# Kernel tuning notes

Measured on AMD Instinct MI355X. Metric: run time of the kernel, lower is better.

## Reference

```python
import jax, jax.numpy as jnp
import numpy as np

C = 512

def _conv1x1(x, w, b):
    # x: [B, C, T], w: [O, C], b: [O] -> [B, O, T]
    return jnp.einsum('oc,bct->bot', w, x) + b[None, :, None]

def setup_inputs() -> dict:
    key = jax.random.key(0)
    ks = jax.random.split(key, 9)
    B, T = 8, 2048
    s = 1.0 / np.sqrt(C)
    inp = {'x': jax.random.normal(ks[0], (B, C, T), dtype=jnp.float32)}
    names = ['theta', 'phi', 'g', 'w']
    for i, n in enumerate(names):
        inp[f'w_{n}'] = jax.random.uniform(ks[1 + 2 * i], (C, C), jnp.float32, -s, s)
        inp[f'b_{n}'] = jax.random.uniform(ks[2 + 2 * i], (C,), jnp.float32, -s, s)
    return inp

def reference(x, w_theta, b_theta, w_phi, b_phi, w_g, b_g, w_w, b_w):
    relu = jax.nn.relu
    feat_theta = relu(_conv1x1(x, w_theta, b_theta))          # [B, C, T]
    feat_phi = relu(_conv1x1(x, w_phi, b_phi))                # [B, C, T]
    # scores: Q^T K over channel dim -> [B, T, T]
    scores = jnp.einsum('bci,bcj->bij', feat_theta, feat_phi)
    attn = jax.nn.softmax(scores, axis=2)                     # [B, T, T]
    feat_g = relu(_conv1x1(x, w_g, b_g))                      # [B, C, T]
    # attention-weighted V: [B, T, T] x [B, T, C] -> [B, T, C] -> [B, C, T]
    feature = jnp.einsum('bij,bcj->bci', attn, feat_g)
    w_feature = relu(_conv1x1(feature, w_w, b_w))
    return w_feature + x
```

## Files before the change

kernel.cpp:

```cpp
#include <hip/hip_runtime.h>
#include <math.h>

#define C_DIM 512
#define T_DIM 2048
#define B_DIM 8

typedef _Float16 f16;
typedef __attribute__((ext_vector_type(8))) _Float16 half8;
typedef __attribute__((ext_vector_type(4))) _Float16 half4;
typedef __attribute__((ext_vector_type(4))) float floatx4;

__global__ __launch_bounds__(256) void convert_w_kernel(
    const float* __restrict__ w0, const float* __restrict__ w1,
    const float* __restrict__ w2, const float* __restrict__ w3,
    f16* __restrict__ o0, f16* __restrict__ o1,
    f16* __restrict__ o2, f16* __restrict__ o3)
{
    const float* src; f16* dst;
    switch (blockIdx.z) {
        case 0:  src = w0; dst = o0; break;
        case 1:  src = w1; dst = o1; break;
        case 2:  src = w2; dst = o2; break;
        default: src = w3; dst = o3; break;
    }
    const int idx = (blockIdx.x * 256 + threadIdx.x) * 4;
    const float4 v = *(const float4*)(src + idx);
    half4 h; h[0] = (f16)v.x; h[1] = (f16)v.y; h[2] = (f16)v.z; h[3] = (f16)v.w;
    *(half4*)(dst + idx) = h;
}

__global__ __launch_bounds__(256) void concat_bias_kernel(
    const float* __restrict__ b0, const float* __restrict__ b1,
    float* __restrict__ o)
{
    const int i = blockIdx.x * 256 + threadIdx.x;
    o[i] = (i < 512) ? b0[i] : b1[i - 512];
}

__global__ __launch_bounds__(256) void transpose_x_kernel(
    const float* __restrict__ x, f16* __restrict__ xt)
{
    __shared__ float xs[32][33];
    const int b  = blockIdx.z;
    const int t0 = blockIdx.x * 32, c0 = blockIdx.y * 32;
    const float* xb = x + (size_t)b * C_DIM * T_DIM;
    const int r = threadIdx.x >> 3, q = threadIdx.x & 7;

    const float4 v = *(const float4*)(xb + (size_t)(c0 + r) * T_DIM + t0 + q * 4);
    xs[r][q * 4 + 0] = v.x; xs[r][q * 4 + 1] = v.y;
    xs[r][q * 4 + 2] = v.z; xs[r][q * 4 + 3] = v.w;
    __syncthreads();

    f16* xtb = xt + (size_t)b * C_DIM * T_DIM;
    half4 h;
    h[0] = (f16)xs[q * 4 + 0][r]; h[1] = (f16)xs[q * 4 + 1][r];
    h[2] = (f16)xs[q * 4 + 2][r]; h[3] = (f16)xs[q * 4 + 3][r];
    *(half4*)(xtb + (size_t)(t0 + r) * C_DIM + c0 + q * 4) = h;
}

__device__ __forceinline__ void gl16(const f16* g, f16* l)
{
    __builtin_amdgcn_global_load_lds(
        (const __attribute__((address_space(1))) unsigned int*)g,
        (__attribute__((address_space(3))) unsigned int*)l,
        16, 0, 0);
}


template<int MODE>
__global__ __launch_bounds__(512, 2) void gemm256(
    const f16* __restrict__ A, size_t sA, int lda,
    const f16* __restrict__ B, size_t sB, int ldb,
    void* __restrict__ Cp, size_t sC, int ldc,
    const float* __restrict__ bias,
    int gx, int K)
{
    __shared__ __align__(16) f16 As[2][2][256 * 32];
    __shared__ __align__(16) f16 Bs[2][2][256 * 32];

    const int f = blockIdx.x;
    const int bz = f & 7;
    const int flat = f >> 3;
    const int jsc = gx >> 2;
    const int sh = (jsc <= 1) ? 0 : (31 - __builtin_clz(jsc));
    const int s = flat >> 4, rem = flat & 15;
    const int i0 = ((s >> sh) * 4 + (rem >> 2)) * 256;
    const int j0 = (((jsc <= 1) ? 0 : (s & (jsc - 1))) * 4 + (rem & 3)) * 256;

    A += (size_t)bz * sA;
    B += (size_t)bz * sB;

    const int tid  = threadIdx.x;
    const int lane = tid & 63;
    const int wave = tid >> 6;
    const int wy = wave >> 2;
    const int wx = wave & 3;
    const int quad = lane >> 4, l16 = lane & 15;

    const int srow = wave * 32 + (lane >> 2);
    const int sch  = (lane & 3) ^ ((lane >> 3) & 3);
    const f16* gA0 = A + (size_t)(i0 + srow) * lda + sch * 8;
    const f16* gA1 = gA0 + (size_t)16 * lda;
    const f16* gB0 = B + (size_t)(j0 + srow) * ldb + sch * 8;
    const f16* gB1 = gB0 + (size_t)16 * ldb;
    const int wsg = wave * 1024;

    const int xq = (quad ^ ((l16 >> 1) & 3)) << 3;
    const int ra = (wy * 128 + l16) * 32 + xq;
    const int rb = (wx * 64 + l16) * 32 + xq;

    const int nt = K >> 6;

#define STAGE_A(t, q) do {                                                    \
        const int off_ = (t) * 64 + (q) * 32;                                 \
        gl16(gA0 + off_, &As[(t) & 1][q][wsg]);                               \
        gl16(gA1 + off_, &As[(t) & 1][q][wsg + 512]);                         \
    } while (0)
#define STAGE_B(t, q) do {                                                    \
        const int off_ = (t) * 64 + (q) * 32;                                 \
        gl16(gB0 + off_, &Bs[(t) & 1][q][wsg]);                               \
        gl16(gB1 + off_, &Bs[(t) & 1][q][wsg + 512]);                         \
    } while (0)
#define PH_MFMA(B0) do {                                                      \
        __builtin_amdgcn_s_setprio(1);                                        \
        _Pragma("unroll")                                                     \
        for (int mi = 0; mi < 4; ++mi) {                                      \
            _Pragma("unroll")                                                 \
            for (int ni = 0; ni < 4; ++ni)                                    \
                acc[(B0) + mi][ni] = __builtin_amdgcn_mfma_f32_16x16x32_f16(  \
                    af[mi], bf[ni], acc[(B0) + mi][ni], 0, 0, 0);             \
        }                                                                     \
        __builtin_amdgcn_s_setprio(0);                                        \
    } while (0)

    STAGE_A(0, 0); STAGE_B(0, 0);
    STAGE_A(0, 1); STAGE_B(0, 1);
    STAGE_A(1, 0); STAGE_B(1, 0);

    floatx4 acc[8][4] = {};

    for (int t = 0; t < nt; ++t) {
        const f16* sa0 = &As[t & 1][0][0];
        const f16* sb0 = &Bs[t & 1][0][0];
        const f16* sa1 = &As[t & 1][1][0];
        const f16* sb1 = &Bs[t & 1][1][0];
        half8 af[4], bf[4];

        if (t + 1 < nt) asm volatile("s_waitcnt vmcnt(8)\ns_barrier" ::: "memory");
        else            asm volatile("s_waitcnt vmcnt(4)\ns_barrier" ::: "memory");
        #pragma unroll
        for (int ni = 0; ni < 4; ++ni) bf[ni] = *(const half8*)&sb0[rb + ni * 512];
        #pragma unroll
        for (int mi = 0; mi < 4; ++mi) af[mi] = *(const half8*)&sa0[ra + mi * 512];
        if (t + 1 < nt) STAGE_A(t + 1, 1);
        PH_MFMA(0);

        #pragma unroll
        for (int mi = 0; mi < 4; ++mi) af[mi] = *(const half8*)&sa0[ra + 2048 + mi * 512];
        if (t + 1 < nt) STAGE_B(t + 1, 1);
        PH_MFMA(4);

        if (t + 1 < nt) asm volatile("s_waitcnt vmcnt(8)\ns_barrier" ::: "memory");
        else            asm volatile("s_waitcnt vmcnt(0)\ns_barrier" ::: "memory");
        #pragma unroll
        for (int ni = 0; ni < 4; ++ni) bf[ni] = *(const half8*)&sb1[rb + ni * 512];
        #pragma unroll
        for (int mi = 0; mi < 4; ++mi) af[mi] = *(const half8*)&sa1[ra + mi * 512];
        if (t + 2 < nt) STAGE_A(t + 2, 0);
        PH_MFMA(0);

        #pragma unroll
        for (int mi = 0; mi < 4; ++mi) af[mi] = *(const half8*)&sa1[ra + 2048 + mi * 512];
        if (t + 2 < nt) STAGE_B(t + 2, 0);
        PH_MFMA(4);
    }
#undef STAGE_A
#undef STAGE_B
#undef PH_MFMA

    #pragma unroll
    for (int m = 0; m < 8; ++m) {
        #pragma unroll
        for (int ni = 0; ni < 4; ++ni) {
            const int col = j0 + wx * 64 + ni * 16 + l16;
            #pragma unroll
            for (int r = 0; r < 4; ++r) {
                const int row = i0 + wy * 128 + m * 16 + quad * 4 + r;
                float v = acc[m][ni][r];
                if (MODE == 1) { v += bias[col]; v = v > 0.f ? v : 0.f; }
                ((f16*)Cp)[(size_t)bz * sC + (size_t)row * ldc + col] = (f16)v;
            }
        }
    }
}

template<int MODE>
__global__ __launch_bounds__(512, 2) void gemm_wide(
    const f16* __restrict__ A, size_t sA, int lda,
    const f16* __restrict__ B, size_t sB, int ldb,
    void* __restrict__ Cp, size_t sC, int ldc,
    const float* __restrict__ bias,
    const float* __restrict__ resid, size_t sR,
    int gxn, int K)
{
    __shared__ __align__(16) f16 As[2][2][128 * 32];
    __shared__ __align__(16) f16 Bs[2][2][256 * 32];

    const int f = blockIdx.x;
    const int bz = f & 7;
    const int inner = f >> 3;
    const int j0 = (inner % gxn) * 256;
    const int i0 = (inner / gxn) * 128;
    A += (size_t)bz * sA;
    B += (size_t)bz * sB;

    const int tid  = threadIdx.x;
    const int lane = tid & 63;
    const int wave = tid >> 6;
    const int wy = wave >> 2;
    const int wx = wave & 3;
    const int quad = lane >> 4, l16 = lane & 15;

    const int sch = (lane & 3) ^ ((lane >> 3) & 3);
    const f16* gA0 = A + (size_t)(i0 + wave * 16 + (lane >> 2)) * lda + sch * 8;
    const f16* gB0 = B + (size_t)(j0 + wave * 32 + (lane >> 2)) * ldb + sch * 8;
    const f16* gB1 = gB0 + (size_t)16 * ldb;

    const int xq = (quad ^ ((l16 >> 1) & 3)) << 3;
    const int ra = (wy * 64 + l16) * 32 + xq;
    const int rb = (wx * 64 + l16) * 32 + xq;

    const int nt = K >> 6;

#define WSTAGE_A(t, q) do {                                                   \
        gl16(gA0 + (t) * 64 + (q) * 32, &As[(t) & 1][q][wave * 512]);         \
    } while (0)
#define WSTAGE_B(t, q) do {                                                   \
        const int off_ = (t) * 64 + (q) * 32;                                 \
        gl16(gB0 + off_, &Bs[(t) & 1][q][wave * 1024]);                       \
        gl16(gB1 + off_, &Bs[(t) & 1][q][wave * 1024 + 512]);                 \
    } while (0)
#define WPH_MFMA() do {                                                       \
        __builtin_amdgcn_s_setprio(1);                                        \
        _Pragma("unroll")                                                     \
        for (int mi = 0; mi < 4; ++mi) {                                      \
            _Pragma("unroll")                                                 \
            for (int ni = 0; ni < 4; ++ni)                                    \
                acc[mi][ni] = __builtin_amdgcn_mfma_f32_16x16x32_f16(         \
                    af[mi], bf[ni], acc[mi][ni], 0, 0, 0);                    \
        }                                                                     \
        __builtin_amdgcn_s_setprio(0);                                        \
    } while (0)

    WSTAGE_A(0, 0); WSTAGE_B(0, 0);
    WSTAGE_A(0, 1); WSTAGE_B(0, 1);
    WSTAGE_A(1, 0); WSTAGE_B(1, 0);

    floatx4 acc[4][4] = {};

    for (int t = 0; t < nt; ++t) {
        const f16* sa0 = &As[t & 1][0][0];
        const f16* sb0 = &Bs[t & 1][0][0];
        const f16* sa1 = &As[t & 1][1][0];
        const f16* sb1 = &Bs[t & 1][1][0];
        half8 af[4], bf[4];

        if (t + 1 < nt) asm volatile("s_waitcnt vmcnt(6)\ns_barrier" ::: "memory");
        else            asm volatile("s_waitcnt vmcnt(3)\ns_barrier" ::: "memory");
        #pragma unroll
        for (int ni = 0; ni < 4; ++ni) bf[ni] = *(const half8*)&sb0[rb + ni * 512];
        #pragma unroll
        for (int mi = 0; mi < 4; ++mi) af[mi] = *(const half8*)&sa0[ra + mi * 512];
        if (t + 1 < nt) { WSTAGE_A(t + 1, 1); WSTAGE_B(t + 1, 1); }
        WPH_MFMA();

        if (t + 1 < nt) asm volatile("s_waitcnt vmcnt(6)\ns_barrier" ::: "memory");
        else            asm volatile("s_waitcnt vmcnt(0)\ns_barrier" ::: "memory");
        #pragma unroll
        for (int ni = 0; ni < 4; ++ni) bf[ni] = *(const half8*)&sb1[rb + ni * 512];
        #pragma unroll
        for (int mi = 0; mi < 4; ++mi) af[mi] = *(const half8*)&sa1[ra + mi * 512];
        if (t + 2 < nt) { WSTAGE_A(t + 2, 0); WSTAGE_B(t + 2, 0); }
        WPH_MFMA();
    }
#undef WSTAGE_A
#undef WSTAGE_B
#undef WPH_MFMA

    #pragma unroll
    for (int mi = 0; mi < 4; ++mi) {
        #pragma unroll
        for (int ni = 0; ni < 4; ++ni) {
            const int col = j0 + wx * 64 + ni * 16 + l16;
            #pragma unroll
            for (int r = 0; r < 4; ++r) {
                const int row = i0 + wy * 64 + mi * 16 + quad * 4 + r;
                float v = acc[mi][ni][r];
                if (MODE == 2) { v += bias[row]; v = v > 0.f ? v : 0.f; }
                if (MODE == 3) {
                    v += bias[row];
                    v = v > 0.f ? v : 0.f;
                    v += resid[(size_t)bz * sR + (size_t)row * ldc + col];
                    ((float*)Cp)[(size_t)bz * sC + (size_t)row * ldc + col] = v;
                } else {
                    ((f16*)Cp)[(size_t)bz * sC + (size_t)row * ldc + col] = (f16)v;
                }
            }
        }
    }
}

__global__ __launch_bounds__(256) void softmax_f16_kernel(f16* __restrict__ S)
{
    const int lane = threadIdx.x & 63;
    f16* p = S + (size_t)(blockIdx.x * 4 + (threadIdx.x >> 6)) * T_DIM;

    half8 h[4];
    float v[32];
    float m = -1e30f;
    #pragma unroll
    for (int u = 0; u < 4; ++u) {
        h[u] = *((const half8*)p + (u * 64 + lane));
        #pragma unroll
        for (int c = 0; c < 8; ++c) {
            v[u * 8 + c] = (float)h[u][c];
            m = fmaxf(m, v[u * 8 + c]);
        }
    }
    #pragma unroll
    for (int off = 32; off; off >>= 1) m = fmaxf(m, __shfl_xor(m, off));

    float s = 0.f;
    #pragma unroll
    for (int i = 0; i < 32; ++i) { v[i] = __expf(v[i] - m); s += v[i]; }
    #pragma unroll
    for (int off = 32; off; off >>= 1) s += __shfl_xor(s, off);
    const float inv = 1.f / s;

    #pragma unroll
    for (int u = 0; u < 4; ++u) {
        #pragma unroll
        for (int c = 0; c < 8; ++c) h[u][c] = (f16)(v[u * 8 + c] * inv);
        *((half8*)p + (u * 64 + lane)) = h[u];
    }
}

extern "C" void kernel_launch(void* const* d_in, const int* in_sizes, int n_in,
                              void* d_out, int out_size, void* d_ws, size_t ws_size,
                              hipStream_t stream)
{
    const float* x       = (const float*)d_in[0];
    const float* w_theta = (const float*)d_in[1];
    const float* b_theta = (const float*)d_in[2];
    const float* w_phi   = (const float*)d_in[3];
    const float* b_phi   = (const float*)d_in[4];
    const float* w_g     = (const float*)d_in[5];
    const float* b_g     = (const float*)d_in[6];
    const float* w_w     = (const float*)d_in[7];
    const float* b_w     = (const float*)d_in[8];
    float* out = (float*)d_out;

    const size_t FE = (size_t)B_DIM * C_DIM * T_DIM;
    const size_t TC = (size_t)T_DIM * C_DIM;
    const size_t TT = (size_t)T_DIM * T_DIM;

    f16* xt      = (f16*)d_ws;
    f16* wtp     = xt + FE;
    f16* wg_h    = wtp + 524288;
    f16* ww_h    = wg_h + 262144;
    float* btp   = (float*)(ww_h + 262144);
    f16* tp      = (f16*)(btp + 1024);
    f16* g       = tp + (size_t)B_DIM * T_DIM * 1024;
    f16* scores  = g + FE;
    f16* feature = tp;

    const dim3 blk(256);
    const dim3 blk512(512);

    convert_w_kernel<<<dim3(256, 1, 4), blk, 0, stream>>>(
        w_theta, w_phi, w_g, w_w, wtp, wtp + 262144, wg_h, ww_h);
    concat_bias_kernel<<<dim3(4), blk, 0, stream>>>(b_theta, b_phi, btp);
    transpose_x_kernel<<<dim3(T_DIM / 32, C_DIM / 32, B_DIM), blk, 0, stream>>>(x, xt);

    gemm256<1><<<dim3(4 * 8 * B_DIM), blk512, 0, stream>>>(
        xt, TC, C_DIM, wtp, 0, C_DIM, tp, (size_t)T_DIM * 1024, 1024,
        btp, 4, C_DIM);
    gemm_wide<2><<<dim3(8 * 4 * B_DIM), blk512, 0, stream>>>(
        wg_h, 0, C_DIM, xt, TC, C_DIM, g, TC, T_DIM, b_g, nullptr, 0,
        8, C_DIM);
    gemm256<0><<<dim3(8 * 8 * B_DIM), blk512, 0, stream>>>(
        tp, (size_t)T_DIM * 1024, 1024, tp + 512, (size_t)T_DIM * 1024, 1024,
        scores, TT, T_DIM, nullptr, 8, C_DIM);
    softmax_f16_kernel<<<dim3(B_DIM * T_DIM / 4), blk, 0, stream>>>(scores);
    gemm_wide<0><<<dim3(2 * 16 * B_DIM), blk512, 0, stream>>>(
        scores, TT, T_DIM, g, TC, T_DIM, feature, TC, C_DIM,
        nullptr, nullptr, 0, 2, T_DIM);
    gemm_wide<3><<<dim3(8 * 4 * B_DIM), blk512, 0, stream>>>(
        ww_h, 0, C_DIM, feature, TC, C_DIM, out, TC, T_DIM, b_w, x, TC,
        8, C_DIM);
}
```

Measured before the change: 258.0 us.

## Fuse softmax into score GEMM epilogue and rescale in attention-V GEMM

Removes the separate softmax kernel. The score GEMM epilogue now computes a per-tile row max, writes exp(s - tile_max) as f16, and stores per-tile (max, sum) stats. The attention-V GEMM reads those stats, rescales each K-tile of A by exp(tile_max - global_max) through registers into LDS, and applies 1/l in its epilogue. This drops one full read and write of the B×T×T score matrix. In exchange, the A operand is staged through registers instead of direct global-to-LDS loads, adds extra vector-ALU work, reuses the wtp workspace for stats, and changes the pipeline wait counts.

```diff
diff --git a/kernel.cpp b/kernel.cpp
--- a/kernel.cpp
+++ b/kernel.cpp
@@ -73,6 +73,7 @@
     const f16* __restrict__ B, size_t sB, int ldb,
     void* __restrict__ Cp, size_t sC, int ldc,
     const float* __restrict__ bias,
+    float2* __restrict__ stats,
     int gx, int K)
 {
     __shared__ __align__(16) f16 As[2][2][256 * 32];
@@ -178,17 +179,73 @@
 #undef STAGE_B
 #undef PH_MFMA
 
-    #pragma unroll
-    for (int m = 0; m < 8; ++m) {
-        #pragma unroll
-        for (int ni = 0; ni < 4; ++ni) {
-            const int col = j0 + wx * 64 + ni * 16 + l16;
+    if constexpr (MODE == 2) {
+        float* red  = (float*)&As[0][0][0];
+        float* mr   = red + 1024;
+        float* red2 = mr + 256;
+        const int jb = j0 >> 8;
+
+        __syncthreads();
+        #pragma unroll
+        for (int m = 0; m < 8; ++m) {
             #pragma unroll
             for (int r = 0; r < 4; ++r) {
-                const int row = i0 + wy * 128 + m * 16 + quad * 4 + r;
-                float v = acc[m][ni][r];
-                if (MODE == 1) { v += bias[col]; v = v > 0.f ? v : 0.f; }
-                ((f16*)Cp)[(size_t)bz * sC + (size_t)row * ldc + col] = (f16)v;
+                float v = fmaxf(fmaxf(acc[m][0][r], acc[m][1][r]),
+                                fmaxf(acc[m][2][r], acc[m][3][r]));
+                v = fmaxf(v, __shfl_xor(v, 1));
+                v = fmaxf(v, __shfl_xor(v, 2));
+                v = fmaxf(v, __shfl_xor(v, 4));
+                v = fmaxf(v, __shfl_xor(v, 8));
+                if (l16 == 0)
+                    red[(wy * 128 + m * 16 + quad * 4 + r) * 4 + wx] = v;
+            }
+        }
+        __syncthreads();
+        if (tid < 256)
+            mr[tid] = fmaxf(fmaxf(red[tid * 4 + 0], red[tid * 4 + 1]),
+                            fmaxf(red[tid * 4 + 2], red[tid * 4 + 3]));
+        __syncthreads();
+        #pragma unroll
+        for (int m = 0; m < 8; ++m) {
+            #pragma unroll
+            for (int r = 0; r < 4; ++r) {
+                const int rl = wy * 128 + m * 16 + quad * 4 + r;
+                const float mrow = mr[rl];
+                float ssum = 0.f;
+                #pragma unroll
+                for (int ni = 0; ni < 4; ++ni) {
+                    const float e = __expf(acc[m][ni][r] - mrow);
+                    ssum += e;
+                    const int col = j0 + wx * 64 + ni * 16 + l16;
+                    ((f16*)Cp)[(size_t)bz * sC + (size_t)(i0 + rl) * ldc + col] = (f16)e;
+                }
+                ssum += __shfl_xor(ssum, 1);
+                ssum += __shfl_xor(ssum, 2);
+                ssum += __shfl_xor(ssum, 4);
+                ssum += __shfl_xor(ssum, 8);
+                if (l16 == 0) red2[rl * 4 + wx] = ssum;
+            }
+        }
+        __syncthreads();
+        if (tid < 256) {
+            const float l = red2[tid * 4 + 0] + red2[tid * 4 + 1]
+                          + red2[tid * 4 + 2] + red2[tid * 4 + 3];
+            stats[((size_t)bz * T_DIM + (i0 + tid)) * 8 + jb] =
+                make_float2(mr[tid], l);
+        }
+    } else {
+        #pragma unroll
+        for (int m = 0; m < 8; ++m) {
+            #pragma unroll
+            for (int ni = 0; ni < 4; ++ni) {
+                const int col = j0 + wx * 64 + ni * 16 + l16;
+                #pragma unroll
+                for (int r = 0; r < 4; ++r) {
+                    const int row = i0 + wy * 128 + m * 16 + quad * 4 + r;
+                    float v = acc[m][ni][r];
+                    if (MODE == 1) { v += bias[col]; v = v > 0.f ? v : 0.f; }
+                    ((f16*)Cp)[(size_t)bz * sC + (size_t)row * ldc + col] = (f16)v;
+                }
             }
         }
     }
@@ -201,10 +258,12 @@
     void* __restrict__ Cp, size_t sC, int ldc,
     const float* __restrict__ bias,
     const float* __restrict__ resid, size_t sR,
+    const float2* __restrict__ stats,
     int gxn, int K)
 {
     __shared__ __align__(16) f16 As[2][2][128 * 32];
     __shared__ __align__(16) f16 Bs[2][2][256 * 32];
+    __shared__ float invl_lds[128];
 
     const int f = blockIdx.x;
     const int bz = f & 7;
@@ -222,7 +281,26 @@
     const int quad = lane >> 4, l16 = lane & 15;
 
     const int sch = (lane & 3) ^ ((lane >> 3) & 3);
-    const f16* gA0 = A + (size_t)(i0 + wave * 16 + (lane >> 2)) * lda + sch * 8;
+    const f16* gA0 = nullptr;
+    const f16* gS  = nullptr;
+    const float2* strow = nullptr;
+    float mrow = 0.f;
+    if constexpr (MODE == 4) {
+        const int rowl = lane >> 2;
+        const int rowg = i0 + wave * 16 + rowl;
+        gS = A + (size_t)rowg * lda + sch * 8;
+        strow = stats + ((size_t)bz * T_DIM + rowg) * 8;
+        mrow = -1e30f;
+        #pragma unroll
+        for (int jb = 0; jb < 8; ++jb) mrow = fmaxf(mrow, strow[jb].x);
+        float lr = 0.f;
+        #pragma unroll
+        for (int jb = 0; jb < 8; ++jb)
+            lr += strow[jb].y * __expf(strow[jb].x - mrow);
+        if ((lane & 3) == 0) invl_lds[wave * 16 + rowl] = 1.f / lr;
+    } else {
+        gA0 = A + (size_t)(i0 + wave * 16 + (lane >> 2)) * lda + sch * 8;
+    }
     const f16* gB0 = B + (size_t)(j0 + wave * 32 + (lane >> 2)) * ldb + sch * 8;
     const f16* gB1 = gB0 + (size_t)16 * ldb;
 
@@ -251,10 +329,31 @@
         }                                                                     \
         __builtin_amdgcn_s_setprio(0);                                        \
     } while (0)
-
-    WSTAGE_A(0, 0); WSTAGE_B(0, 0);
-    WSTAGE_A(0, 1); WSTAGE_B(0, 1);
-    WSTAGE_A(1, 0); WSTAGE_B(1, 0);
+#define LAEX(T, q, D, M) do {                                                 \
+        D = *(const half8*)(gS + (T) * 64 + (q) * 32);                        \
+        M = strow[(T) >> 2].x;                                                \
+    } while (0)
+#define WAEX(T, q, D, M) do {                                                 \
+        const float sc_ = __expf((M) - mrow);                                 \
+        const f16 sh_ = (f16)sc_;                                             \
+        const half8 vs_ = {sh_, sh_, sh_, sh_, sh_, sh_, sh_, sh_};           \
+        *(half8*)&As[(T) & 1][q][wave * 512 + lane * 8] = (D) * vs_;          \
+    } while (0)
+
+    half8 pA0, pA1; float pm0 = 0.f, pm1 = 0.f;
+
+    if constexpr (MODE == 4) {
+        half8 a00, a01, a10, a11;
+        LAEX(0, 0, a00, pm0); LAEX(0, 1, a01, pm0);
+        LAEX(1, 0, a10, pm0); LAEX(1, 1, a11, pm0);
+        WAEX(0, 0, a00, pm0); WAEX(0, 1, a01, pm0);
+        WAEX(1, 0, a10, pm0); WAEX(1, 1, a11, pm0);
+        WSTAGE_B(0, 0); WSTAGE_B(0, 1); WSTAGE_B(1, 0);
+    } else {
+        WSTAGE_A(0, 0); WSTAGE_B(0, 0);
+        WSTAGE_A(0, 1); WSTAGE_B(0, 1);
+        WSTAGE_A(1, 0); WSTAGE_B(1, 0);
+    }
 
     floatx4 acc[4][4] = {};
 
@@ -265,27 +364,59 @@
         const f16* sb1 = &Bs[t & 1][1][0];
         half8 af[4], bf[4];
 
-        if (t + 1 < nt) asm volatile("s_waitcnt vmcnt(6)\ns_barrier" ::: "memory");
-        else            asm volatile("s_waitcnt vmcnt(3)\ns_barrier" ::: "memory");
+        if constexpr (MODE == 4) {
+            if (t == 0)
+                asm volatile("s_waitcnt vmcnt(4) lgkmcnt(0)\ns_barrier" ::: "memory");
+            else if (t < nt - 2)
+                asm volatile("s_waitcnt vmcnt(8) lgkmcnt(0)\ns_barrier" ::: "memory");
+            else
+                asm volatile("s_waitcnt vmcnt(0) lgkmcnt(0)\ns_barrier" ::: "memory");
+        } else {
+            if (t + 1 < nt) asm volatile("s_waitcnt vmcnt(6)\ns_barrier" ::: "memory");
+            else            asm volatile("s_waitcnt vmcnt(3)\ns_barrier" ::: "memory");
+        }
         #pragma unroll
         for (int ni = 0; ni < 4; ++ni) bf[ni] = *(const half8*)&sb0[rb + ni * 512];
         #pragma unroll
         for (int mi = 0; mi < 4; ++mi) af[mi] = *(const half8*)&sa0[ra + mi * 512];
-        if (t + 1 < nt) { WSTAGE_A(t + 1, 1); WSTAGE_B(t + 1, 1); }
+        if constexpr (MODE == 4) {
+            if (t >= 1 && t + 1 < nt) WAEX(t + 1, 0, pA0, pm0);
+            if (t + 2 < nt) LAEX(t + 2, 0, pA0, pm0);
+        } else {
+            if (t + 1 < nt) WSTAGE_A(t + 1, 1);
+        }
+        if (t + 1 < nt) WSTAGE_B(t + 1, 1);
         WPH_MFMA();
 
-        if (t + 1 < nt) asm volatile("s_waitcnt vmcnt(6)\ns_barrier" ::: "memory");
-        else            asm volatile("s_waitcnt vmcnt(0)\ns_barrier" ::: "memory");
+        if constexpr (MODE == 4) {
+            if (t == 0)
+                asm volatile("s_waitcnt vmcnt(6) lgkmcnt(0)\ns_barrier" ::: "memory");
+            else if (t < nt - 2)
+                asm volatile("s_waitcnt vmcnt(8) lgkmcnt(0)\ns_barrier" ::: "memory");
+            else
+                asm volatile("s_waitcnt vmcnt(0) lgkmcnt(0)\ns_barrier" ::: "memory");
+        } else {
+            if (t + 1 < nt) asm volatile("s_waitcnt vmcnt(6)\ns_barrier" ::: "memory");
+            else            asm volatile("s_waitcnt vmcnt(0)\ns_barrier" ::: "memory");
+        }
         #pragma unroll
         for (int ni = 0; ni < 4; ++ni) bf[ni] = *(const half8*)&sb1[rb + ni * 512];
         #pragma unroll
         for (int mi = 0; mi < 4; ++mi) af[mi] = *(const half8*)&sa1[ra + mi * 512];
-        if (t + 2 < nt) { WSTAGE_A(t + 2, 0); WSTAGE_B(t + 2, 0); }
+        if constexpr (MODE == 4) {
+            if (t >= 1 && t + 1 < nt) WAEX(t + 1, 1, pA1, pm1);
+            if (t + 2 < nt) LAEX(t + 2, 1, pA1, pm1);
+        } else {
+            if (t + 2 < nt) WSTAGE_A(t + 2, 0);
+        }
+        if (t + 2 < nt) WSTAGE_B(t + 2, 0);
         WPH_MFMA();
     }
 #undef WSTAGE_A
 #undef WSTAGE_B
 #undef WPH_MFMA
+#undef LAEX
+#undef WAEX
 
     #pragma unroll
     for (int mi = 0; mi < 4; ++mi) {
@@ -294,9 +425,11 @@
             const int col = j0 + wx * 64 + ni * 16 + l16;
             #pragma unroll
             for (int r = 0; r < 4; ++r) {
-                const int row = i0 + wy * 64 + mi * 16 + quad * 4 + r;
+                const int rl = wy * 64 + mi * 16 + quad * 4 + r;
+                const int row = i0 + rl;
                 float v = acc[mi][ni][r];
                 if (MODE == 2) { v += bias[row]; v = v > 0.f ? v : 0.f; }
+                if (MODE == 4) { v *= invl_lds[rl]; }
                 if (MODE == 3) {
                     v += bias[row];
                     v = v > 0.f ? v : 0.f;
@@ -307,41 +440,6 @@
                 }
             }
         }
-    }
-}
-
-__global__ __launch_bounds__(256) void softmax_f16_kernel(f16* __restrict__ S)
-{
-    const int lane = threadIdx.x & 63;
-    f16* p = S + (size_t)(blockIdx.x * 4 + (threadIdx.x >> 6)) * T_DIM;
-
-    half8 h[4];
-    float v[32];
-    float m = -1e30f;
-    #pragma unroll
-    for (int u = 0; u < 4; ++u) {
-        h[u] = *((const half8*)p + (u * 64 + lane));
-        #pragma unroll
-        for (int c = 0; c < 8; ++c) {
-            v[u * 8 + c] = (float)h[u][c];
-            m = fmaxf(m, v[u * 8 + c]);
-        }
-    }
-    #pragma unroll
-    for (int off = 32; off; off >>= 1) m = fmaxf(m, __shfl_xor(m, off));
-
-    float s = 0.f;
-    #pragma unroll
-    for (int i = 0; i < 32; ++i) { v[i] = __expf(v[i] - m); s += v[i]; }
-    #pragma unroll
-    for (int off = 32; off; off >>= 1) s += __shfl_xor(s, off);
-    const float inv = 1.f / s;
-
-    #pragma unroll
-    for (int u = 0; u < 4; ++u) {
-        #pragma unroll
-        for (int c = 0; c < 8; ++c) h[u][c] = (f16)(v[u * 8 + c] * inv);
-        *((half8*)p + (u * 64 + lane)) = h[u];
     }
 }
 
@@ -373,6 +471,7 @@
     f16* g       = tp + (size_t)B_DIM * T_DIM * 1024;
     f16* scores  = g + FE;
     f16* feature = tp;
+    float2* stats = (float2*)wtp;
 
     const dim3 blk(256);
     const dim3 blk512(512);
@@ -384,18 +483,17 @@
 
     gemm256<1><<<dim3(4 * 8 * B_DIM), blk512, 0, stream>>>(
         xt, TC, C_DIM, wtp, 0, C_DIM, tp, (size_t)T_DIM * 1024, 1024,
-        btp, 4, C_DIM);
+        btp, nullptr, 4, C_DIM);
     gemm_wide<2><<<dim3(8 * 4 * B_DIM), blk512, 0, stream>>>(
         wg_h, 0, C_DIM, xt, TC, C_DIM, g, TC, T_DIM, b_g, nullptr, 0,
-        8, C_DIM);
-    gemm256<0><<<dim3(8 * 8 * B_DIM), blk512, 0, stream>>>(
+        nullptr, 8, C_DIM);
+    gemm256<2><<<dim3(8 * 8 * B_DIM), blk512, 0, stream>>>(
         tp, (size_t)T_DIM * 1024, 1024, tp + 512, (size_t)T_DIM * 1024, 1024,
-        scores, TT, T_DIM, nullptr, 8, C_DIM);
-    softmax_f16_kernel<<<dim3(B_DIM * T_DIM / 4), blk, 0, stream>>>(scores);
-    gemm_wide<0><<<dim3(2 * 16 * B_DIM), blk512, 0, stream>>>(
+        scores, TT, T_DIM, nullptr, stats, 8, C_DIM);
+    gemm_wide<4><<<dim3(2 * 16 * B_DIM), blk512, 0, stream>>>(
         scores, TT, T_DIM, g, TC, T_DIM, feature, TC, C_DIM,
-        nullptr, nullptr, 0, 2, T_DIM);
+        nullptr, nullptr, 0, stats, 2, T_DIM);
     gemm_wide<3><<<dim3(8 * 4 * B_DIM), blk512, 0, stream>>>(
         ww_h, 0, C_DIM, feature, TC, C_DIM, out, TC, T_DIM, b_w, x, TC,
-        8, C_DIM);
-}
+        nullptr, 8, C_DIM);
+}
```

Result: no change. 262.0 us (+1.5%).
